# Optimization experiments

Measured on AMD Instinct MI355X. Metric: run time of the kernel, lower is better.

## Reference

```python
import jax, jax.numpy as jnp
import numpy as np

WINDOW_SIZE = 11
SIGMA = 1.5
C1 = 0.01 ** 2
C2 = 0.03 ** 2


def _gaussian_window(channel, dtype):
    # 1D gaussian, normalized, then outer product -> 2D window, expanded per channel
    xs = np.arange(WINDOW_SIZE) - WINDOW_SIZE // 2
    g = np.exp(-(xs.astype(np.float64) ** 2) / (2.0 * SIGMA ** 2))
    g = (g / g.sum()).astype(np.float32)
    w2d = np.outer(g, g)  # [ws, ws]
    w = np.broadcast_to(w2d[None, None], (channel, 1, WINDOW_SIZE, WINDOW_SIZE))
    return jnp.asarray(w, dtype=dtype)


def _depthwise_conv(img, window, channel):
    pad = WINDOW_SIZE // 2
    return jax.lax.conv_general_dilated(
        img, window,
        window_strides=(1, 1),
        padding=[(pad, pad), (pad, pad)],
        dimension_numbers=('NCHW', 'OIHW', 'NCHW'),
        feature_group_count=channel)


def setup_inputs() -> dict:
    key = jax.random.key(0)
    k1, k2 = jax.random.split(key)
    shape = (16, 3, 512, 512)
    x = jax.random.uniform(k1, shape, dtype=jnp.float32)
    y = jax.random.uniform(k2, shape, dtype=jnp.float32)
    return {"x": x, "y": y}


def reference(x, y):
    channel = x.shape[-3]
    window = _gaussian_window(channel, x.dtype)

    mu1 = _depthwise_conv(x, window, channel)
    mu2 = _depthwise_conv(y, window, channel)
    mu1_sq = mu1 * mu1
    mu2_sq = mu2 * mu2
    mu1_mu2 = mu1 * mu2
    sigma1_sq = _depthwise_conv(x * x, window, channel) - mu1_sq
    sigma2_sq = _depthwise_conv(y * y, window, channel) - mu2_sq
    sigma12 = _depthwise_conv(x * y, window, channel) - mu1_mu2

    ssim_map = ((2.0 * mu1_mu2 + C1) * (2.0 * sigma12 + C2)) / (
        (mu1_sq + mu2_sq + C1) * (sigma1_sq + sigma2_sq + C2))
    # DSSIM = 1 - mean(ssim)
    return 1.0 - jnp.mean(ssim_map)
```

## Files before the change

kernel.cpp:

```cpp
#include <hip/hip_runtime.h>


typedef float f32x2 __attribute__((ext_vector_type(2)));

#define IMG_W   512
#define IMG_H   512
#define NPLANES 48

#define TW 256
#define TH 32
#define ROWSV (TH + 10)
#define LW 272
#define NCHUNK 4
#define GX (IMG_W / TW)
#define GY (IMG_H / TH)
#define NBLK (GX * GY * NPLANES)

__global__ __launch_bounds__(256, 4)
void dssim_main(const float* __restrict__ xin, const float* __restrict__ yin,
                float* __restrict__ partial) {
    __shared__ f32x2 ls[11][LW];
    __shared__ float wpart[4];

    const int t   = threadIdx.x;
    const int tx0 = blockIdx.x * TW;
    const int ty0 = blockIdx.y * TH;
    const size_t pbase = (size_t)blockIdx.z * (IMG_W * IMG_H);
    const int base4 = (tx0 >> 2) - 2;
    const float* __restrict__ xp = xin + pbase;
    const float* __restrict__ yp = yin + pbase;

    float g[11];
    {
        float s = 0.f;
#pragma unroll
        for (int i = 0; i < 11; ++i) {
            float d = (float)(i - 5);
            g[i] = expf(-(d * d) * (1.0f / 4.5f));
            s += g[i];
        }
        float inv = 1.0f / s;
#pragma unroll
        for (int i = 0; i < 11; ++i) g[i] *= inv;
    }

    const float C1 = 0.0001f, C2 = 0.0009f;

    f32x2 rA[11], rS[11];
    float lsum = 0.f;

    for (int c = 0; c < NCHUNK; ++c) {
        const int c0 = c * 11;

        __syncthreads();
        for (int idx = t; idx < 11 * 68; idx += 256) {
            const int j   = idx / 68;
            const int c4  = idx - j * 68;
            const int i   = c0 + j;
            const int gr  = ty0 - 5 + i;
            const int gc4 = base4 + c4;
            float4 xv = make_float4(0.f, 0.f, 0.f, 0.f);
            float4 yv = make_float4(0.f, 0.f, 0.f, 0.f);
            if (i < ROWSV && gr >= 0 && gr < IMG_H && gc4 >= 0 && gc4 < (IMG_W / 4)) {
                const size_t o = (size_t)gr * IMG_W + (gc4 << 2);
                xv = *(const float4*)(xp + o);
                yv = *(const float4*)(yp + o);
            }
            float4 a, b;
            a.x = xv.x + yv.x; a.y = xv.x - yv.x;
            a.z = xv.y + yv.y; a.w = xv.y - yv.y;
            b.x = xv.z + yv.z; b.y = xv.z - yv.z;
            b.z = xv.w + yv.w; b.w = xv.w - yv.w;
            *(float4*)&ls[j][(c4 << 2)]     = a;
            *(float4*)&ls[j][(c4 << 2) + 2] = b;
        }
        __syncthreads();

#pragma unroll
        for (int j = 0; j < 11; ++j) {
            const int i = c0 + j;
            if (i < ROWSV) {
                f32x2 ha = {0.f, 0.f};
                f32x2 hp = {0.f, 0.f};
#pragma unroll
                for (int k = 0; k < 11; ++k) {
                    const f32x2 v = ls[j][t + 3 + k];
                    const f32x2 gk2 = {g[k], g[k]};
                    ha = __builtin_elementwise_fma(gk2, v, ha);
                    hp = __builtin_elementwise_fma(gk2 * v, v, hp);
                }
                rA[j] = ha; rS[j] = hp;

                if (i >= 10) {
                    f32x2 A2 = {0.f, 0.f};
                    f32x2 S2 = {0.f, 0.f};
#pragma unroll
                    for (int k = 0; k < 11; ++k) {
                        const int s = (j + 1 + k) % 11;
                        const f32x2 gk2 = {g[k], g[k]};
                        A2 = __builtin_elementwise_fma(gk2, rA[s], A2);
                        S2 = __builtin_elementwise_fma(gk2, rS[s], S2);
                    }
                    const float U = A2.x, W = A2.y, P = S2.x, Q = S2.y;
                    const float U2 = U * U;
                    const float W2 = W * W;
                    const float A  = 0.5f * (U2 + W2);
                    const float B  = 0.5f * (U2 - W2);
                    const float den2 = fmaf(0.5f, P + Q, -A) + C2;
                    const float num2 = fmaf(0.5f, P - Q, -B) + C2;
                    lsum += (B + C1) * num2 *
                            __builtin_amdgcn_rcpf((A + C1) * den2);
                }
            }
        }
    }

#pragma unroll
    for (int off = 32; off >= 1; off >>= 1)
        lsum += __shfl_down(lsum, off, 64);
    if ((t & 63) == 0) wpart[t >> 6] = lsum;
    __syncthreads();
    if (t == 0) {
        partial[((size_t)blockIdx.z * GY + blockIdx.y) * GX + blockIdx.x] =
            wpart[0] + wpart[1] + wpart[2] + wpart[3];
    }
}

__global__ __launch_bounds__(256)
void dssim_final(const float* __restrict__ partial, float* __restrict__ out) {
    __shared__ double wsum[4];
    double s = 0.0;
    for (int i = threadIdx.x; i < NBLK; i += 256) s += (double)partial[i];
#pragma unroll
    for (int off = 32; off >= 1; off >>= 1)
        s += __shfl_down(s, off, 64);
    if ((threadIdx.x & 63) == 0) wsum[threadIdx.x >> 6] = s;
    __syncthreads();
    if (threadIdx.x == 0) {
        const double tot = wsum[0] + wsum[1] + wsum[2] + wsum[3];
        out[0] = (float)(1.0 - tot / 12582912.0);
    }
}

extern "C" void kernel_launch(void* const* d_in, const int* in_sizes, int n_in,
                              void* d_out, int out_size, void* d_ws, size_t ws_size,
                              hipStream_t stream) {
    const float* x = (const float*)d_in[0];
    const float* y = (const float*)d_in[1];
    float* out = (float*)d_out;
    float* partial = (float*)d_ws;

    dim3 grid(GX, GY, NPLANES);
    dim3 block(256);
    dssim_main<<<grid, block, 0, stream>>>(x, y, partial);
    dssim_final<<<1, block, 0, stream>>>(partial, out);
}
```

Before: 55.14 us.

## Compute separable Gaussian blurs with fp16 MFMA banded-matrix products

Replaces the scalar FMA horizontal and vertical 11-tap convolutions with 16x16x32 fp16 MFMA products against banded Gaussian weight matrices. Inputs are stored as fp16 sum/difference planes in LDS. Each block now handles a 16-row full-width strip with a per-wave LDS transpose between the horizontal and vertical passes. This moves the convolution work onto the matrix units to cut VALU cost, but fp16 storage of inputs, squares and intermediates reduces precision. It also recomputes many zero band entries.

```diff
diff --git a/kernel.cpp b/kernel.cpp
--- a/kernel.cpp
+++ b/kernel.cpp
@@ -1,127 +1,172 @@
 #include <hip/hip_runtime.h>
 
 
-typedef float f32x2 __attribute__((ext_vector_type(2)));
+typedef _Float16 half8 __attribute__((ext_vector_type(8)));
+typedef _Float16 half4v __attribute__((ext_vector_type(4)));
+typedef float f32x4 __attribute__((ext_vector_type(4)));
 
 #define IMG_W   512
 #define IMG_H   512
 #define NPLANES 48
-
-#define TW 256
-#define TH 32
-#define ROWSV (TH + 10)
-#define LW 272
-#define NCHUNK 4
-#define GX (IMG_W / TW)
-#define GY (IMG_H / TH)
-#define NBLK (GX * GY * NPLANES)
-
-__global__ __launch_bounds__(256, 4)
+#define BR      16
+#define RAWROWS 26
+#define RAWP    528
+#define TP      40
+#define GRX     (IMG_H / BR)
+#define NBLK    (GRX * NPLANES)
+
+__global__ __launch_bounds__(256, 2)
 void dssim_main(const float* __restrict__ xin, const float* __restrict__ yin,
                 float* __restrict__ partial) {
-    __shared__ f32x2 ls[11][LW];
+    __shared__ _Float16 rawU[RAWROWS][RAWP];
+    __shared__ _Float16 rawW[RAWROWS][RAWP];
+    __shared__ _Float16 ldsT[4][4][16][TP];
     __shared__ float wpart[4];
 
-    const int t   = threadIdx.x;
-    const int tx0 = blockIdx.x * TW;
-    const int ty0 = blockIdx.y * TH;
-    const size_t pbase = (size_t)blockIdx.z * (IMG_W * IMG_H);
-    const int base4 = (tx0 >> 2) - 2;
+    const int t    = threadIdx.x;
+    const int lane = t & 63;
+    const int wid  = t >> 6;
+    const int bn   = lane & 15;
+    const int jg   = lane >> 4;
+    const int r0   = blockIdx.x * BR;
+    const size_t pbase = (size_t)blockIdx.y * (IMG_W * IMG_H);
     const float* __restrict__ xp = xin + pbase;
     const float* __restrict__ yp = yin + pbase;
 
-    float g[11];
+    float ginv;
     {
         float s = 0.f;
 #pragma unroll
         for (int i = 0; i < 11; ++i) {
             float d = (float)(i - 5);
-            g[i] = expf(-(d * d) * (1.0f / 4.5f));
-            s += g[i];
-        }
-        float inv = 1.0f / s;
-#pragma unroll
-        for (int i = 0; i < 11; ++i) g[i] *= inv;
-    }
+            s += expf(-(d * d) * (1.0f / 4.5f));
+        }
+        ginv = 1.0f / s;
+    }
+
+    half8 whF, wvF;
+#pragma unroll
+    for (int j = 0; j < 8; ++j) {
+        const int k = 8 * jg + j;
+        const int dh = k - bn - 3;
+        const int dv = k - bn;
+        float wh = 0.f, wv = 0.f;
+        if (dh >= 0 && dh < 11) {
+            const float d = (float)(dh - 5);
+            wh = ginv * expf(-(d * d) * (1.0f / 4.5f));
+        }
+        if (dv >= 0 && dv < 11) {
+            const float d = (float)(dv - 5);
+            wv = ginv * expf(-(d * d) * (1.0f / 4.5f));
+        }
+        whF[j] = (_Float16)wh;
+        wvF[j] = (_Float16)wv;
+    }
+
+    if (t < 104) {
+        const int rr   = t >> 2;
+        const int hw   = (t >> 1) & 1;
+        const int side = t & 1;
+        _Float16* base = hw ? &rawW[rr][0] : &rawU[rr][0];
+        *(half8*)(base + (side ? (RAWP - 8) : 0)) = (half8)(_Float16)0.0f;
+    }
+
+#pragma unroll
+    for (int it = 0; it < 13; ++it) {
+        const int idx = t + (it << 8);
+        const int rr  = idx >> 7;
+        const int c4  = idx & 127;
+        const int gr  = r0 - 5 + rr;
+        float4 xv = make_float4(0.f, 0.f, 0.f, 0.f);
+        float4 yv = make_float4(0.f, 0.f, 0.f, 0.f);
+        if (gr >= 0 && gr < IMG_H) {
+            const size_t o = (size_t)gr * IMG_W + (c4 << 2);
+            xv = *(const float4*)(xp + o);
+            yv = *(const float4*)(yp + o);
+        }
+        half4v u, w;
+        u[0] = (_Float16)(xv.x + yv.x); w[0] = (_Float16)(xv.x - yv.x);
+        u[1] = (_Float16)(xv.y + yv.y); w[1] = (_Float16)(xv.y - yv.y);
+        u[2] = (_Float16)(xv.z + yv.z); w[2] = (_Float16)(xv.z - yv.z);
+        u[3] = (_Float16)(xv.w + yv.w); w[3] = (_Float16)(xv.w - yv.w);
+        *(half4v*)&rawU[rr][8 + (c4 << 2)] = u;
+        *(half4v*)&rawW[rr][8 + (c4 << 2)] = w;
+    }
+    __syncthreads();
 
     const float C1 = 0.0001f, C2 = 0.0009f;
-
-    f32x2 rA[11], rS[11];
+    const f32x4 zf = {0.f, 0.f, 0.f, 0.f};
     float lsum = 0.f;
 
-    for (int c = 0; c < NCHUNK; ++c) {
-        const int c0 = c * 11;
-
-        __syncthreads();
-        for (int idx = t; idx < 11 * 68; idx += 256) {
-            const int j   = idx / 68;
-            const int c4  = idx - j * 68;
-            const int i   = c0 + j;
-            const int gr  = ty0 - 5 + i;
-            const int gc4 = base4 + c4;
-            float4 xv = make_float4(0.f, 0.f, 0.f, 0.f);
-            float4 yv = make_float4(0.f, 0.f, 0.f, 0.f);
-            if (i < ROWSV && gr >= 0 && gr < IMG_H && gc4 >= 0 && gc4 < (IMG_W / 4)) {
-                const size_t o = (size_t)gr * IMG_W + (gc4 << 2);
-                xv = *(const float4*)(xp + o);
-                yv = *(const float4*)(yp + o);
+    for (int i = 0; i < 8; ++i) {
+        const int c0 = (wid + 4 * i) << 4;
+
+#pragma unroll
+        for (int rt = 0; rt < 2; ++rt) {
+            const int rr = 16 * rt + bn;
+            const bool valid = rr < RAWROWS;
+            const int rrc = valid ? rr : 0;
+            half8 aU = *(const half8*)&rawU[rrc][c0 + 8 * jg];
+            half8 aW = *(const half8*)&rawW[rrc][c0 + 8 * jg];
+            if (!valid) {
+                aU = (half8)(_Float16)0.0f;
+                aW = (half8)(_Float16)0.0f;
             }
-            float4 a, b;
-            a.x = xv.x + yv.x; a.y = xv.x - yv.x;
-            a.z = xv.y + yv.y; a.w = xv.y - yv.y;
-            b.x = xv.z + yv.z; b.y = xv.z - yv.z;
-            b.z = xv.w + yv.w; b.w = xv.w - yv.w;
-            *(float4*)&ls[j][(c4 << 2)]     = a;
-            *(float4*)&ls[j][(c4 << 2) + 2] = b;
-        }
-        __syncthreads();
-
-#pragma unroll
-        for (int j = 0; j < 11; ++j) {
-            const int i = c0 + j;
-            if (i < ROWSV) {
-                f32x2 ha = {0.f, 0.f};
-                f32x2 hp = {0.f, 0.f};
-#pragma unroll
-                for (int k = 0; k < 11; ++k) {
-                    const f32x2 v = ls[j][t + 3 + k];
-                    const f32x2 gk2 = {g[k], g[k]};
-                    ha = __builtin_elementwise_fma(gk2, v, ha);
-                    hp = __builtin_elementwise_fma(gk2 * v, v, hp);
-                }
-                rA[j] = ha; rS[j] = hp;
-
-                if (i >= 10) {
-                    f32x2 A2 = {0.f, 0.f};
-                    f32x2 S2 = {0.f, 0.f};
-#pragma unroll
-                    for (int k = 0; k < 11; ++k) {
-                        const int s = (j + 1 + k) % 11;
-                        const f32x2 gk2 = {g[k], g[k]};
-                        A2 = __builtin_elementwise_fma(gk2, rA[s], A2);
-                        S2 = __builtin_elementwise_fma(gk2, rS[s], S2);
-                    }
-                    const float U = A2.x, W = A2.y, P = S2.x, Q = S2.y;
-                    const float U2 = U * U;
-                    const float W2 = W * W;
-                    const float A  = 0.5f * (U2 + W2);
-                    const float B  = 0.5f * (U2 - W2);
-                    const float den2 = fmaf(0.5f, P + Q, -A) + C2;
-                    const float num2 = fmaf(0.5f, P - Q, -B) + C2;
-                    lsum += (B + C1) * num2 *
-                            __builtin_amdgcn_rcpf((A + C1) * den2);
-                }
+            half8 aU2, aW2;
+#pragma unroll
+            for (int d = 0; d < 8; ++d) {
+                aU2[d] = aU[d] * aU[d];
+                aW2[d] = aW[d] * aW[d];
             }
+            const f32x4 cU  = __builtin_amdgcn_mfma_f32_16x16x32_f16(aU,  whF, zf, 0, 0, 0);
+            const f32x4 cW  = __builtin_amdgcn_mfma_f32_16x16x32_f16(aW,  whF, zf, 0, 0, 0);
+            const f32x4 cU2 = __builtin_amdgcn_mfma_f32_16x16x32_f16(aU2, whF, zf, 0, 0, 0);
+            const f32x4 cW2 = __builtin_amdgcn_mfma_f32_16x16x32_f16(aW2, whF, zf, 0, 0, 0);
+
+            half4v hU, hW, hU2, hW2;
+#pragma unroll
+            for (int ii = 0; ii < 4; ++ii) {
+                hU[ii]  = (_Float16)cU[ii];
+                hW[ii]  = (_Float16)cW[ii];
+                hU2[ii] = (_Float16)cU2[ii];
+                hW2[ii] = (_Float16)cW2[ii];
+            }
+            const int kk = 16 * rt + 4 * jg;
+            *(half4v*)&ldsT[wid][0][bn][kk] = hU;
+            *(half4v*)&ldsT[wid][1][bn][kk] = hW;
+            *(half4v*)&ldsT[wid][2][bn][kk] = hU2;
+            *(half4v*)&ldsT[wid][3][bn][kk] = hW2;
+        }
+
+        const half8 aTU  = *(const half8*)&ldsT[wid][0][bn][8 * jg];
+        const half8 aTW  = *(const half8*)&ldsT[wid][1][bn][8 * jg];
+        const half8 aTU2 = *(const half8*)&ldsT[wid][2][bn][8 * jg];
+        const half8 aTW2 = *(const half8*)&ldsT[wid][3][bn][8 * jg];
+        const f32x4 accU = __builtin_amdgcn_mfma_f32_16x16x32_f16(aTU,  wvF, zf, 0, 0, 0);
+        const f32x4 accW = __builtin_amdgcn_mfma_f32_16x16x32_f16(aTW,  wvF, zf, 0, 0, 0);
+        const f32x4 accP = __builtin_amdgcn_mfma_f32_16x16x32_f16(aTU2, wvF, zf, 0, 0, 0);
+        const f32x4 accQ = __builtin_amdgcn_mfma_f32_16x16x32_f16(aTW2, wvF, zf, 0, 0, 0);
+
+#pragma unroll
+        for (int ii = 0; ii < 4; ++ii) {
+            const float U = accU[ii], W = accW[ii];
+            const float P = accP[ii], Q = accQ[ii];
+            const float U2 = U * U, W2 = W * W;
+            const float A = 0.5f * (U2 + W2);
+            const float B = 0.5f * (U2 - W2);
+            const float den2 = fmaf(0.5f, P + Q, -A) + C2;
+            const float num2 = fmaf(0.5f, P - Q, -B) + C2;
+            lsum += (B + C1) * num2 * __builtin_amdgcn_rcpf((A + C1) * den2);
         }
     }
 
 #pragma unroll
     for (int off = 32; off >= 1; off >>= 1)
         lsum += __shfl_down(lsum, off, 64);
-    if ((t & 63) == 0) wpart[t >> 6] = lsum;
+    if (lane == 0) wpart[wid] = lsum;
     __syncthreads();
     if (t == 0) {
-        partial[((size_t)blockIdx.z * GY + blockIdx.y) * GX + blockIdx.x] =
+        partial[(size_t)blockIdx.y * GRX + blockIdx.x] =
             wpart[0] + wpart[1] + wpart[2] + wpart[3];
     }
 }
@@ -150,7 +195,7 @@
     float* out = (float*)d_out;
     float* partial = (float*)d_ws;
 
-    dim3 grid(GX, GY, NPLANES);
+    dim3 grid(GRX, NPLANES);
     dim3 block(256);
     dssim_main<<<grid, block, 0, stream>>>(x, y, partial);
     dssim_final<<<1, block, 0, stream>>>(partial, out);
```

Measured after the change: 56.97 us. +3.3%, slower.
